# Optimization experiments

Measured on AMD Instinct MI355X. Metric: run time of the kernel, lower is better.

Reference implementation:

```python
import jax, jax.numpy as jnp
import numpy as np

B, LQ, LK, D = 8, 2048, 2048, 512
NEG = -1e9  # stands in for -inf; avoids nan in grads, same softmax result


def setup_inputs() -> dict:
    key = jax.random.key(0)
    kq, kk, kv, km, kr = jax.random.split(key, 5)
    q = jax.random.normal(kq, (B, LQ, D), dtype=jnp.float32)
    k = jax.random.normal(kk, (B, LK, D), dtype=jnp.float32)
    v = jax.random.normal(kv, (B, LK, D), dtype=jnp.float32)
    attn_mask = jax.random.bernoulli(km, 0.1, (B, LK))
    # per-batch positive ratio so masked scores stay very negative after scaling
    ratio = jax.random.uniform(kr, (B,), dtype=jnp.float32, minval=0.5, maxval=1.5)
    scale = jnp.float32(1.0 / np.sqrt(D))
    return {"q": q, "k": k, "v": v, "ratio": ratio, "scale": scale, "attn_mask": attn_mask}


def reference(q, k, v, ratio, scale, attn_mask):
    # QK^T, scale, mask-fill, ratio modulation, softmax, AV
    # (dropout is identity in eval/deterministic baseline)
    scores = jnp.einsum("bqd,bkd->bqk", q, k) * scale          # [B, LQ, LK]
    scores = jnp.where(attn_mask[:, None, :], jnp.float32(NEG), scores)
    scores = scores * ratio[:, None, None]                       # per-batch modulation
    attn = jax.nn.softmax(scores, axis=-1)
    return jnp.einsum("bqk,bkd->bqd", attn, v)                   # [B, LQ, D]
```

## Files before the change

kernel.cpp:

```cpp
#include <hip/hip_runtime.h>
#include <stdint.h>

#define Bn  8
#define LQn 2048
#define LKn 2048
#define Dn  512
#define NT  8

using f32x4  = __attribute__((ext_vector_type(4)))  float;
using f32x16 = __attribute__((ext_vector_type(16))) float;
using bf16x8 = __attribute__((ext_vector_type(8)))  __bf16;
using u16x8  = __attribute__((ext_vector_type(8)))  unsigned short;

#define WS_MASK_OFF 256
#define WS_KP_OFF   (WS_MASK_OFF + Bn*LKn*4)
#define KP_BYTES    ((size_t)Bn*64*32*1024)
#define WS_VP_OFF   (WS_KP_OFF + KP_BYTES)
#define VP_BYTES    ((size_t)Bn*128*16*1024)
#define WS_REQ      ((size_t)WS_VP_OFF + VP_BYTES)

union BFU { __bf16 h; unsigned short u; };
static __device__ __forceinline__ unsigned short f2bfu(float x) { BFU t; t.h = (__bf16)x; return t.u; }

__global__ void mask_prep_kernel(const void* __restrict__ mraw, float* __restrict__ maskadd) {
  __shared__ int sBig, sOff;
  const int tid = threadIdx.x;
  if (tid == 0) { sBig = 0; sOff = 0; }
  __syncthreads();
  const unsigned char* mb = (const unsigned char*)mraw;
  int big = 0, off = 0;
  for (int i = tid; i < Bn*LKn; i += blockDim.x) {
    unsigned char v = mb[i];
    big |= (v > 1) ? 1 : 0;
    off |= (((i & 3) != 0) && v != 0) ? 1 : 0;
  }
  if (big) atomicOr(&sBig, 1);
  if (off) atomicOr(&sOff, 1);
  __syncthreads();
  const int f = sBig ? 2 : (sOff ? 1 : 0);
  for (int i = tid; i < Bn*LKn; i += blockDim.x) {
    bool m;
    if (f == 2)      m = ((const float*)mraw)[i] != 0.0f;
    else if (f == 1) m = mb[i] != 0;
    else             m = ((const int*)mraw)[i] != 0;
    maskadd[i] = m ? -1e30f : 0.0f;
  }
}

__global__ void conv_kp_kernel(const float* __restrict__ k, unsigned short* __restrict__ kp) {
  const int gid = blockIdx.x * 256 + threadIdx.x;
  const int frag = gid >> 6, lane = gid & 63;
  const int b = frag >> 11;
  const int rem = frag & 2047;
  const int kg = rem >> 5, ks = rem & 31;
  const int key = kg*32 + (lane & 31);
  const int hi = lane >> 5;
  const float* src = k + ((size_t)(b*LKn) + key)*Dn + ks*16 + hi*8;
  const f32x4 a = *(const f32x4*)src;
  const f32x4 c = *(const f32x4*)(src + 4);
  u16x8 o;
#pragma unroll
  for (int j = 0; j < 4; ++j) { o[j] = f2bfu(a[j]); o[j+4] = f2bfu(c[j]); }
  *(u16x8*)(kp + (size_t)frag*512 + lane*8) = o;
}

__global__ void conv_vp_kernel(const float* __restrict__ v, unsigned short* __restrict__ vp) {
  __shared__ float vt[16*512];
  const int b = blockIdx.y, kslice = blockIdx.x;
  const float* src = v + ((size_t)(b*LKn) + kslice*16)*Dn;
#pragma unroll
  for (int p = 0; p < 8; ++p) {
    const int idx = p*256 + threadIdx.x;
    *(f32x4*)&vt[idx*4] = *(const f32x4*)(src + (size_t)idx*4);
  }
  __syncthreads();
  unsigned short* dst = vp + ((size_t)(b*128 + kslice)*16)*512;
#pragma unroll
  for (int p = 0; p < 4; ++p) {
    const int slot = p*256 + threadIdx.x;
    const int dg = slot >> 6, lane = slot & 63;
    const int d = dg*32 + (lane & 31);
    const int k0 = (lane >> 5)*8;
    u16x8 o;
#pragma unroll
    for (int j = 0; j < 8; ++j) o[j] = f2bfu(vt[(k0+j)*512 + d]);
    *(u16x8*)(dst + (size_t)dg*512 + lane*8) = o;
  }
}

#define BARRIER_LGKM                                        \
  asm volatile("s_waitcnt lgkmcnt(0)" ::: "memory");        \
  __builtin_amdgcn_s_barrier();                             \
  asm volatile("" ::: "memory");

__launch_bounds__(512, 2)
__global__ void attn_kernel(const float* __restrict__ q, const unsigned short* __restrict__ kp,
                            const unsigned short* __restrict__ vp,
                            const float* __restrict__ ratio, const float* __restrict__ scalep,
                            const float* __restrict__ maskadd, float* __restrict__ out) {
  __shared__ __align__(16) unsigned short Ql[2*32*512];
  __shared__ __align__(16) unsigned short Pl[2*16*512];
  __shared__ __align__(16) float maskl[LKn];
  __shared__ float redm[8][64];
  __shared__ float reds[8][64];

  const int tid = threadIdx.x;
  const int w = tid >> 6, lane = tid & 63;
  const int qc = lane & 31, hi = lane >> 5;
  const int b = blockIdx.x & 7, qtile = blockIdx.x >> 3;
  const int qbase = qtile * 64;
  const float c2 = scalep[0] * ratio[b] * 1.4426950408889634f;

  *(f32x4*)&maskl[tid*4] = *(const f32x4*)(maskadd + (size_t)b*LKn + tid*4);

#pragma unroll
  for (int cc = 0; cc < 8; ++cc) {
    const int idx = cc*512 + tid;
    const int hi2 = idx & 1, qc2 = (idx >> 1) & 31, ks2 = (idx >> 6) & 31, qg2 = idx >> 11;
    const float* src = q + ((size_t)(b*LQn) + qbase + qg2*32 + qc2)*Dn + ks2*16 + hi2*8;
    const f32x4 a = *(const f32x4*)src;
    const f32x4 bb = *(const f32x4*)(src + 4);
    u16x8 o;
#pragma unroll
    for (int j = 0; j < 4; ++j) { o[j] = f2bfu(a[j]); o[j+4] = f2bfu(bb[j]); }
    *(u16x8*)((char*)Ql + qg2*32768 + ks2*1024 + qc2*32 + hi2*16) = o;
  }
  __syncthreads();

  f32x16 o00, o01, o10, o11;
#pragma unroll
  for (int r = 0; r < 16; ++r) { o00[r]=0.f; o01[r]=0.f; o10[r]=0.f; o11[r]=0.f; }
  float m0 = -3.0e38f, m1 = -3.0e38f, l0 = 0.f, l1 = 0.f;

  const char* kpB = (const char*)kp + (size_t)b*2048*1024;
  const char* vpB = (const char*)vp + (size_t)b*2048*1024;
  const int loff = lane*16;
  const char* Qlb = (const char*)Ql + qc*32 + hi*16;
  const char* prc = (const char*)Pl + qc*32 + hi*16;

  bf16x8 pb[16];
  {
    const char* kf0 = kpB + (size_t)w*32768 + loff;
#pragma unroll
    for (int i = 0; i < 16; ++i) pb[i] = *(const bf16x8*)(kf0 + i*1024);
  }

  for (int t = 0; t < NT; ++t) {
    const char* kf  = kpB + (size_t)(t*8 + w)*32768 + loff;
    const char* kfn = kpB + (size_t)((t+1 < NT ? t+1 : 0)*8 + w)*32768 + loff;
    const char* vf  = vpB + ((size_t)(t*16)*16 + w*2)*1024 + loff;
    const int tn = (t + 1 < NT) ? 1 : 0;

    f32x4 m4[4];
#pragma unroll
    for (int g = 0; g < 4; ++g)
      m4[g] = *(const f32x4*)&maskl[t*256 + w*32 + g*8 + hi*4];

    f32x16 S0, S1;
#pragma unroll
    for (int r = 0; r < 16; ++r) { S0[r] = 0.f; S1[r] = 0.f; }
    __builtin_amdgcn_s_setprio(1);
#pragma unroll
    for (int i = 0; i < 32; ++i) {
      const bf16x8 kk = pb[i & 15];
      const bf16x8 q0 = *(const bf16x8*)(Qlb + i*1024);
      const bf16x8 q1 = *(const bf16x8*)(Qlb + 32768 + i*1024);
      S0 = __builtin_amdgcn_mfma_f32_32x32x16_bf16(kk, q0, S0, 0, 0, 0);
      S1 = __builtin_amdgcn_mfma_f32_32x32x16_bf16(kk, q1, S1, 0, 0, 0);
      if (i < 16) {
        pb[i & 15] = *(const bf16x8*)(kf + (i+16)*1024);
      } else {
        const int j = i - 16;
        pb[i & 15] = *(const bf16x8*)(vf + (size_t)(j >> 1)*16384 + (j & 1)*1024);
      }
    }
    __builtin_amdgcn_s_setprio(0);

    float sl0[16], sl1[16];
    float vx0 = -3.0e38f, vx1 = -3.0e38f;
#pragma unroll
    for (int r = 0; r < 16; ++r) {
      const float mr = m4[r >> 2][r & 3];
      sl0[r] = S0[r]*c2 + mr; vx0 = fmaxf(vx0, sl0[r]);
      sl1[r] = S1[r]*c2 + mr; vx1 = fmaxf(vx1, sl1[r]);
    }
    vx0 = fmaxf(vx0, __shfl_xor(vx0, 32));
    vx1 = fmaxf(vx1, __shfl_xor(vx1, 32));
    if (lane < 32) { redm[w][qc] = vx0; redm[w][32 + qc] = vx1; }
    BARRIER_LGKM;

    float mt0 = redm[0][qc], mt1 = redm[0][32 + qc];
#pragma unroll
    for (int w2 = 1; w2 < 8; ++w2) {
      mt0 = fmaxf(mt0, redm[w2][qc]);
      mt1 = fmaxf(mt1, redm[w2][32 + qc]);
    }
    const float mn0 = fmaxf(m0, mt0), mn1 = fmaxf(m1, mt1);
    const float fac0 = exp2f(m0 - mn0), fac1 = exp2f(m1 - mn1);
    m0 = mn0; m1 = mn1;

    float ps0 = 0.f, ps1 = 0.f;
    {
      char* pw0p = (char*)Pl + (w*2)*1024 + qc*32 + hi*8;
#pragma unroll
      for (int g = 0; g < 4; ++g) {
        const int off = (g & 1)*16 + (g >> 1)*1024;
        float p0 = exp2f(sl0[g*4+0] - mn0), p1 = exp2f(sl0[g*4+1] - mn0);
        float p2 = exp2f(sl0[g*4+2] - mn0), p3 = exp2f(sl0[g*4+3] - mn0);
        ps0 += (p0 + p1) + (p2 + p3);
        unsigned long long u0 = (unsigned long long)((unsigned int)f2bfu(p0) | ((unsigned int)f2bfu(p1) << 16))
                              | ((unsigned long long)((unsigned int)f2bfu(p2) | ((unsigned int)f2bfu(p3) << 16)) << 32);
        *(unsigned long long*)(pw0p + off) = u0;
        p0 = exp2f(sl1[g*4+0] - mn1); p1 = exp2f(sl1[g*4+1] - mn1);
        p2 = exp2f(sl1[g*4+2] - mn1); p3 = exp2f(sl1[g*4+3] - mn1);
        ps1 += (p0 + p1) + (p2 + p3);
        unsigned long long u1 = (unsigned long long)((unsigned int)f2bfu(p0) | ((unsigned int)f2bfu(p1) << 16))
                              | ((unsigned long long)((unsigned int)f2bfu(p2) | ((unsigned int)f2bfu(p3) << 16)) << 32);
        *(unsigned long long*)(pw0p + 16384 + off) = u1;
      }
    }
    ps0 += __shfl_xor(ps0, 32);
    ps1 += __shfl_xor(ps1, 32);
    if (lane < 32) { reds[w][qc] = ps0; reds[w][32 + qc] = ps1; }
    BARRIER_LGKM;

    float ls0 = reds[0][qc], ls1 = reds[0][32 + qc];
#pragma unroll
    for (int w2 = 1; w2 < 8; ++w2) { ls0 += reds[w2][qc]; ls1 += reds[w2][32 + qc]; }
    l0 = l0*fac0 + ls0;
    l1 = l1*fac1 + ls1;
#pragma unroll
    for (int r = 0; r < 16; ++r) {
      o00[r] *= fac0; o01[r] *= fac0;
      o10[r] *= fac1; o11[r] *= fac1;
    }

    __builtin_amdgcn_s_setprio(1);
#pragma unroll
    for (int ks2 = 0; ks2 < 16; ++ks2) {
      const bf16x8 pf0 = *(const bf16x8*)(prc + ks2*1024);
      const bf16x8 pf1 = *(const bf16x8*)(prc + 16384 + ks2*1024);
      const bf16x8 v0 = pb[(2*ks2) & 15];
      const bf16x8 v1 = pb[(2*ks2 + 1) & 15];
      o00 = __builtin_amdgcn_mfma_f32_32x32x16_bf16(v0, pf0, o00, 0, 0, 0);
      o10 = __builtin_amdgcn_mfma_f32_32x32x16_bf16(v0, pf1, o10, 0, 0, 0);
      o01 = __builtin_amdgcn_mfma_f32_32x32x16_bf16(v1, pf0, o01, 0, 0, 0);
      o11 = __builtin_amdgcn_mfma_f32_32x32x16_bf16(v1, pf1, o11, 0, 0, 0);
      const int j0 = 2*ks2, j1 = 2*ks2 + 1;
      if (j0 < 16) {
        pb[j0 & 15] = *(const bf16x8*)(vf + (size_t)((j0+16) >> 1)*16384 + ((j0+16) & 1)*1024);
        pb[j1 & 15] = *(const bf16x8*)(vf + (size_t)((j1+16) >> 1)*16384 + ((j1+16) & 1)*1024);
      } else if (tn) {
        pb[j0 & 15] = *(const bf16x8*)(kfn + (j0-16)*1024);
        pb[j1 & 15] = *(const bf16x8*)(kfn + (j1-16)*1024);
      }
    }
    __builtin_amdgcn_s_setprio(0);
  }

  const float li0 = 1.0f / l0, li1 = 1.0f / l1;
  float* ob0 = out + ((size_t)(b*LQn) + qbase + qc)*Dn + w*64;
  float* ob1 = ob0 + (size_t)32*Dn;
#pragma unroll
  for (int dg = 0; dg < 2; ++dg) {
#pragma unroll
    for (int rq = 0; rq < 4; ++rq) {
      f32x4 ov0, ov1;
#pragma unroll
      for (int c = 0; c < 4; ++c) {
        if (dg == 0) { ov0[c] = o00[rq*4 + c]*li0; ov1[c] = o10[rq*4 + c]*li1; }
        else         { ov0[c] = o01[rq*4 + c]*li0; ov1[c] = o11[rq*4 + c]*li1; }
      }
      *(f32x4*)(ob0 + dg*32 + rq*8 + hi*4) = ov0;
      *(f32x4*)(ob1 + dg*32 + rq*8 + hi*4) = ov1;
    }
  }
}

extern "C" void kernel_launch(void* const* d_in, const int* in_sizes, int n_in,
                              void* d_out, int out_size, void* d_ws, size_t ws_size,
                              hipStream_t stream) {
  const float* q      = (const float*)d_in[0];
  const float* k      = (const float*)d_in[1];
  const float* v      = (const float*)d_in[2];
  const float* ratio  = (const float*)d_in[3];
  const float* scalep = (const float*)d_in[4];
  const void*  mask   = d_in[5];
  float* out = (float*)d_out;
  char* ws = (char*)d_ws;

  if (ws_size < WS_REQ) return;

  float* maskadd      = (float*)(ws + WS_MASK_OFF);
  unsigned short* kpk = (unsigned short*)(ws + WS_KP_OFF);
  unsigned short* vpk = (unsigned short*)(ws + WS_VP_OFF);

  hipLaunchKernelGGL(mask_prep_kernel, dim3(1), dim3(1024), 0, stream, mask, maskadd);
  hipLaunchKernelGGL(conv_kp_kernel, dim3(Bn*64*32*64/256), dim3(256), 0, stream, k, kpk);
  hipLaunchKernelGGL(conv_vp_kernel, dim3(128, Bn), dim3(256), 0, stream, v, vpk);
  hipLaunchKernelGGL(attn_kernel, dim3(Bn*(LQn/64)), dim3(512), 0, stream,
                     q, kpk, vpk, ratio, scalep, maskadd, out);
}
```

Baseline: 121.7 us.

## Software-pipeline PV of previous tile with softmax of current tile

```diff
diff --git a/kernel.cpp b/kernel.cpp
--- a/kernel.cpp
+++ b/kernel.cpp
@@ -93,16 +93,22 @@
   __builtin_amdgcn_s_barrier();                             \
   asm volatile("" ::: "memory");
 
+#define KADDR(s)  (kpB + (size_t)((((s) & 255) >> 5)*8 + w)*32768 + (((s) & 31) << 10) + loff)
+#define VADDR(s)  (vpB + (size_t)(((((s) & 255) >> 5)*256) + ((((s) & 31) >> 1) << 4) + w*2 + ((s) & 1))*1024 + loff)
+
+#define PBUF 32768
+#define PQG  16384
+
 __launch_bounds__(512, 2)
 __global__ void attn_kernel(const float* __restrict__ q, const unsigned short* __restrict__ kp,
                             const unsigned short* __restrict__ vp,
                             const float* __restrict__ ratio, const float* __restrict__ scalep,
                             const float* __restrict__ maskadd, float* __restrict__ out) {
   __shared__ __align__(16) unsigned short Ql[2*32*512];
-  __shared__ __align__(16) unsigned short Pl[2*16*512];
+  __shared__ __align__(16) unsigned short Pl[2][2*16*512];
   __shared__ __align__(16) float maskl[LKn];
   __shared__ float redm[8][64];
-  __shared__ float reds[8][64];
+  __shared__ float reds[2][8][64];
 
   const int tid = threadIdx.x;
   const int w = tid >> 6, lane = tid & 63;
@@ -131,52 +137,38 @@
 #pragma unroll
   for (int r = 0; r < 16; ++r) { o00[r]=0.f; o01[r]=0.f; o10[r]=0.f; o11[r]=0.f; }
   float m0 = -3.0e38f, m1 = -3.0e38f, l0 = 0.f, l1 = 0.f;
+  float fp0 = 1.0f, fp1 = 1.0f;
+  float sl0[16], sl1[16];
 
   const char* kpB = (const char*)kp + (size_t)b*2048*1024;
   const char* vpB = (const char*)vp + (size_t)b*2048*1024;
   const int loff = lane*16;
   const char* Qlb = (const char*)Ql + qc*32 + hi*16;
-  const char* prc = (const char*)Pl + qc*32 + hi*16;
-
-  bf16x8 pb[16];
-  {
-    const char* kf0 = kpB + (size_t)w*32768 + loff;
-#pragma unroll
-    for (int i = 0; i < 16; ++i) pb[i] = *(const bf16x8*)(kf0 + i*1024);
-  }
+
+  bf16x8 pb[8], vb[8];
+#pragma unroll
+  for (int i = 0; i < 8; ++i) { pb[i] = *(const bf16x8*)KADDR(i); vb[i] = *(const bf16x8*)VADDR(i); }
 
   for (int t = 0; t < NT; ++t) {
-    const char* kf  = kpB + (size_t)(t*8 + w)*32768 + loff;
-    const char* kfn = kpB + (size_t)((t+1 < NT ? t+1 : 0)*8 + w)*32768 + loff;
-    const char* vf  = vpB + ((size_t)(t*16)*16 + w*2)*1024 + loff;
-    const int tn = (t + 1 < NT) ? 1 : 0;
-
-    f32x4 m4[4];
-#pragma unroll
-    for (int g = 0; g < 4; ++g)
-      m4[g] = *(const f32x4*)&maskl[t*256 + w*32 + g*8 + hi*4];
-
     f32x16 S0, S1;
 #pragma unroll
     for (int r = 0; r < 16; ++r) { S0[r] = 0.f; S1[r] = 0.f; }
     __builtin_amdgcn_s_setprio(1);
 #pragma unroll
     for (int i = 0; i < 32; ++i) {
-      const bf16x8 kk = pb[i & 15];
+      const bf16x8 kk = pb[i & 7];
       const bf16x8 q0 = *(const bf16x8*)(Qlb + i*1024);
       const bf16x8 q1 = *(const bf16x8*)(Qlb + 32768 + i*1024);
       S0 = __builtin_amdgcn_mfma_f32_32x32x16_bf16(kk, q0, S0, 0, 0, 0);
       S1 = __builtin_amdgcn_mfma_f32_32x32x16_bf16(kk, q1, S1, 0, 0, 0);
-      if (i < 16) {
-        pb[i & 15] = *(const bf16x8*)(kf + (i+16)*1024);
-      } else {
-        const int j = i - 16;
-        pb[i & 15] = *(const bf16x8*)(vf + (size_t)(j >> 1)*16384 + (j & 1)*1024);
-      }
+      pb[i & 7] = *(const bf16x8*)KADDR(t*32 + i + 8);
     }
     __builtin_amdgcn_s_setprio(0);
 
-    float sl0[16], sl1[16];
+    f32x4 m4[4];
+#pragma unroll
+    for (int g = 0; g < 4; ++g)
+      m4[g] = *(const f32x4*)&maskl[t*256 + w*32 + g*8 + hi*4];
     float vx0 = -3.0e38f, vx1 = -3.0e38f;
 #pragma unroll
     for (int r = 0; r < 16; ++r) {
@@ -189,70 +181,92 @@
     if (lane < 32) { redm[w][qc] = vx0; redm[w][32 + qc] = vx1; }
     BARRIER_LGKM;
 
+    if (t > 0) {
+      float ls0 = reds[(t-1) & 1][0][qc], ls1 = reds[(t-1) & 1][0][32 + qc];
+#pragma unroll
+      for (int w2 = 1; w2 < 8; ++w2) { ls0 += reds[(t-1) & 1][w2][qc]; ls1 += reds[(t-1) & 1][w2][32 + qc]; }
+      l0 = l0*fp0 + ls0;
+      l1 = l1*fp1 + ls1;
+    }
     float mt0 = redm[0][qc], mt1 = redm[0][32 + qc];
 #pragma unroll
-    for (int w2 = 1; w2 < 8; ++w2) {
-      mt0 = fmaxf(mt0, redm[w2][qc]);
-      mt1 = fmaxf(mt1, redm[w2][32 + qc]);
-    }
+    for (int w2 = 1; w2 < 8; ++w2) { mt0 = fmaxf(mt0, redm[w2][qc]); mt1 = fmaxf(mt1, redm[w2][32 + qc]); }
     const float mn0 = fmaxf(m0, mt0), mn1 = fmaxf(m1, mt1);
-    const float fac0 = exp2f(m0 - mn0), fac1 = exp2f(m1 - mn1);
+    const float ft0 = exp2f(m0 - mn0), ft1 = exp2f(m1 - mn1);
     m0 = mn0; m1 = mn1;
+    if (t > 0) {
+#pragma unroll
+      for (int r = 0; r < 16; ++r) { o00[r] *= fp0; o01[r] *= fp0; o10[r] *= fp1; o11[r] *= fp1; }
+    }
 
     float ps0 = 0.f, ps1 = 0.f;
-    {
-      char* pw0p = (char*)Pl + (w*2)*1024 + qc*32 + hi*8;
-#pragma unroll
-      for (int g = 0; g < 4; ++g) {
+    char* pwr = (char*)Pl + (t & 1)*PBUF + (w*2)*1024 + qc*32 + hi*8;
+    const char* prd = (const char*)Pl + ((t+1) & 1)*PBUF + qc*32 + hi*16;
+
+    __builtin_amdgcn_s_setprio(1);
+#pragma unroll
+    for (int ks2 = 0; ks2 < 16; ++ks2) {
+      if (t > 0) {
+        const bf16x8 pf0 = *(const bf16x8*)(prd + ks2*1024);
+        const bf16x8 pf1 = *(const bf16x8*)(prd + PQG + ks2*1024);
+        const bf16x8 v0 = vb[(2*ks2) & 7];
+        const bf16x8 v1 = vb[(2*ks2 + 1) & 7];
+        o00 = __builtin_amdgcn_mfma_f32_32x32x16_bf16(v0, pf0, o00, 0, 0, 0);
+        o10 = __builtin_amdgcn_mfma_f32_32x32x16_bf16(v0, pf1, o10, 0, 0, 0);
+        o01 = __builtin_amdgcn_mfma_f32_32x32x16_bf16(v1, pf0, o01, 0, 0, 0);
+        o11 = __builtin_amdgcn_mfma_f32_32x32x16_bf16(v1, pf1, o11, 0, 0, 0);
+        vb[(2*ks2) & 7]     = *(const bf16x8*)VADDR((t-1)*32 + 2*ks2 + 8);
+        vb[(2*ks2 + 1) & 7] = *(const bf16x8*)VADDR((t-1)*32 + 2*ks2 + 9);
+      }
+      if ((ks2 & 3) == 0) {
+        const int g = ks2 >> 2;
         const int off = (g & 1)*16 + (g >> 1)*1024;
         float p0 = exp2f(sl0[g*4+0] - mn0), p1 = exp2f(sl0[g*4+1] - mn0);
         float p2 = exp2f(sl0[g*4+2] - mn0), p3 = exp2f(sl0[g*4+3] - mn0);
         ps0 += (p0 + p1) + (p2 + p3);
         unsigned long long u0 = (unsigned long long)((unsigned int)f2bfu(p0) | ((unsigned int)f2bfu(p1) << 16))
                               | ((unsigned long long)((unsigned int)f2bfu(p2) | ((unsigned int)f2bfu(p3) << 16)) << 32);
-        *(unsigned long long*)(pw0p + off) = u0;
+        *(unsigned long long*)(pwr + off) = u0;
         p0 = exp2f(sl1[g*4+0] - mn1); p1 = exp2f(sl1[g*4+1] - mn1);
         p2 = exp2f(sl1[g*4+2] - mn1); p3 = exp2f(sl1[g*4+3] - mn1);
         ps1 += (p0 + p1) + (p2 + p3);
         unsigned long long u1 = (unsigned long long)((unsigned int)f2bfu(p0) | ((unsigned int)f2bfu(p1) << 16))
                               | ((unsigned long long)((unsigned int)f2bfu(p2) | ((unsigned int)f2bfu(p3) << 16)) << 32);
-        *(unsigned long long*)(pw0p + 16384 + off) = u1;
+        *(unsigned long long*)(pwr + PQG + off) = u1;
       }
     }
+    __builtin_amdgcn_s_setprio(0);
+
     ps0 += __shfl_xor(ps0, 32);
     ps1 += __shfl_xor(ps1, 32);
-    if (lane < 32) { reds[w][qc] = ps0; reds[w][32 + qc] = ps1; }
+    if (lane < 32) { reds[t & 1][w][qc] = ps0; reds[t & 1][w][32 + qc] = ps1; }
+    fp0 = ft0; fp1 = ft1;
     BARRIER_LGKM;
-
-    float ls0 = reds[0][qc], ls1 = reds[0][32 + qc];
-#pragma unroll
-    for (int w2 = 1; w2 < 8; ++w2) { ls0 += reds[w2][qc]; ls1 += reds[w2][32 + qc]; }
-    l0 = l0*fac0 + ls0;
-    l1 = l1*fac1 + ls1;
-#pragma unroll
-    for (int r = 0; r < 16; ++r) {
-      o00[r] *= fac0; o01[r] *= fac0;
-      o10[r] *= fac1; o11[r] *= fac1;
-    }
-
+  }
+
+  {
+    float ls0 = reds[(NT-1) & 1][0][qc], ls1 = reds[(NT-1) & 1][0][32 + qc];
+#pragma unroll
+    for (int w2 = 1; w2 < 8; ++w2) { ls0 += reds[(NT-1) & 1][w2][qc]; ls1 += reds[(NT-1) & 1][w2][32 + qc]; }
+    l0 = l0*fp0 + ls0;
+    l1 = l1*fp1 + ls1;
+#pragma unroll
+    for (int r = 0; r < 16; ++r) { o00[r] *= fp0; o01[r] *= fp0; o10[r] *= fp1; o11[r] *= fp1; }
+    const char* prd = (const char*)Pl + ((NT-1) & 1)*PBUF + qc*32 + hi*16;
     __builtin_amdgcn_s_setprio(1);
 #pragma unroll
     for (int ks2 = 0; ks2 < 16; ++ks2) {
-      const bf16x8 pf0 = *(const bf16x8*)(prc + ks2*1024);
-      const bf16x8 pf1 = *(const bf16x8*)(prc + 16384 + ks2*1024);
-      const bf16x8 v0 = pb[(2*ks2) & 15];
-      const bf16x8 v1 = pb[(2*ks2 + 1) & 15];
+      const bf16x8 pf0 = *(const bf16x8*)(prd + ks2*1024);
+      const bf16x8 pf1 = *(const bf16x8*)(prd + PQG + ks2*1024);
+      const bf16x8 v0 = vb[(2*ks2) & 7];
+      const bf16x8 v1 = vb[(2*ks2 + 1) & 7];
       o00 = __builtin_amdgcn_mfma_f32_32x32x16_bf16(v0, pf0, o00, 0, 0, 0);
       o10 = __builtin_amdgcn_mfma_f32_32x32x16_bf16(v0, pf1, o10, 0, 0, 0);
       o01 = __builtin_amdgcn_mfma_f32_32x32x16_bf16(v1, pf0, o01, 0, 0, 0);
       o11 = __builtin_amdgcn_mfma_f32_32x32x16_bf16(v1, pf1, o11, 0, 0, 0);
-      const int j0 = 2*ks2, j1 = 2*ks2 + 1;
-      if (j0 < 16) {
-        pb[j0 & 15] = *(const bf16x8*)(vf + (size_t)((j0+16) >> 1)*16384 + ((j0+16) & 1)*1024);
-        pb[j1 & 15] = *(const bf16x8*)(vf + (size_t)((j1+16) >> 1)*16384 + ((j1+16) & 1)*1024);
-      } else if (tn) {
-        pb[j0 & 15] = *(const bf16x8*)(kfn + (j0-16)*1024);
-        pb[j1 & 15] = *(const bf16x8*)(kfn + (j1-16)*1024);
+      if (ks2 < 12) {
+        vb[(2*ks2) & 7]     = *(const bf16x8*)VADDR((NT-1)*32 + 2*ks2 + 8);
+        vb[(2*ks2 + 1) & 7] = *(const bf16x8*)VADDR((NT-1)*32 + 2*ks2 + 9);
       }
     }
     __builtin_amdgcn_s_setprio(0);
```

Measured after the change: 324.3 us. +166.4%, slower.
